# Kernel optimization log

Hardware: AMD Instinct MI355X
Metric: run time of the kernel (lower is better)

The kernel has to match this reference:

```python
import jax, jax.numpy as jnp
import numpy as np

N = 50000
E = 800000
EPS = 1e-5
GAT_SLOPE = 0.2   # PyG GATConv internal LeakyReLU slope
ACT_SLOPE = 0.01  # decoder's LeakyReLU(alpha)


def setup_inputs() -> dict:
    key = jax.random.key(0)
    ks = jax.random.split(key, 10)
    d = {
        "embeddings": jax.random.normal(ks[0], (N, 64), jnp.float32),
        "edge_index": jax.random.randint(ks[1], (2, E), 0, N, jnp.int64),
        "W1": jax.random.normal(ks[2], (64, 128), jnp.float32) * 0.1,
        "a_src1": jax.random.normal(ks[3], (128,), jnp.float32) * 0.1,
        "a_dst1": jax.random.normal(ks[4], (128,), jnp.float32) * 0.1,
        "b1": jnp.zeros((128,), jnp.float32),
        "gamma1": jnp.ones((128,), jnp.float32),
        "beta1": jnp.zeros((128,), jnp.float32),
        "W2": jax.random.normal(ks[5], (128, 256), jnp.float32) * 0.1,
        "a_src2": jax.random.normal(ks[6], (256,), jnp.float32) * 0.1,
        "a_dst2": jax.random.normal(ks[7], (256,), jnp.float32) * 0.1,
        "b2": jnp.zeros((256,), jnp.float32),
        "gamma2": jnp.ones((256,), jnp.float32),
        "beta2": jnp.zeros((256,), jnp.float32),
        "Wf": jax.random.normal(ks[8], (256, 256), jnp.float32) * 0.1,
        "bf": jnp.zeros((256,), jnp.float32),
    }
    return d


def gat_conv(x, src, dst, W, a_s, a_d, b):
    # PyG GATConv, heads=1, concat=False, add_self_loops=True (loops appended in caller)
    h = x @ W                                    # [N, out]
    e = h @ a_s                                  # alpha_src per node
    f = h @ a_d                                  # alpha_dst per node
    logits = jax.nn.leaky_relu(e[src] + f[dst], GAT_SLOPE)   # [E']
    # scatter-softmax over destination neighborhoods
    m = jax.ops.segment_max(logits, dst, num_segments=N)
    ex = jnp.exp(logits - m[dst])
    denom = jax.ops.segment_sum(ex, dst, num_segments=N)
    alpha = ex / denom[dst]                      # [E']
    out = jax.ops.segment_sum(h[src] * alpha[:, None], dst, num_segments=N)
    return out + b


def batch_norm(x, gamma, beta):
    mu = jnp.mean(x, axis=0)
    var = jnp.mean((x - mu) ** 2, axis=0)        # biased, as torch BN uses
    return (x - mu) * jax.lax.rsqrt(var + EPS) * gamma + beta


def reference(embeddings, edge_index, W1, a_src1, a_dst1, b1, gamma1, beta1,
              W2, a_src2, a_dst2, b2, gamma2, beta2, Wf, bf):
    loops = jnp.arange(N, dtype=edge_index.dtype)
    src = jnp.concatenate([edge_index[0], loops])
    dst = jnp.concatenate([edge_index[1], loops])
    x = embeddings
    for (W, a_s, a_d, b, g, be) in [
        (W1, a_src1, a_dst1, b1, gamma1, beta1),
        (W2, a_src2, a_dst2, b2, gamma2, beta2),
    ]:
        x = gat_conv(x, src, dst, W, a_s, a_d, b)
        x = batch_norm(x, g, be)
        x = jax.nn.leaky_relu(x, ACT_SLOPE)
        # dropout: identity (eval mode)
    return x @ Wf + bf
```

## Files before the change

### kernel.cpp

```cpp
#include <hip/hip_runtime.h>
#include <hip/hip_fp16.h>
#include <math.h>

#define N_NODES 50000
#define N_EDGES 800000
#define N_TOT   850000
#define EPS_BN  1e-5f
#define GAT_SLOPE 0.2f
#define ACT_SLOPE 0.01f
#define NBUCK   ((N_NODES + 255) / 256)
#define BCAP    5120
#define K1_CH   4096
#define K1_NB   ((N_TOT + K1_CH - 1) / K1_CH)
#define GB64    ((N_NODES + 63) / 64)

typedef _Float16 half8_t __attribute__((ext_vector_type(8)));
typedef _Float16 half4_t __attribute__((ext_vector_type(4)));
typedef _Float16 half2_t __attribute__((ext_vector_type(2)));
typedef float    f32x4   __attribute__((ext_vector_type(4)));

__device__ __forceinline__ float wred_max(float x) {
#pragma unroll
    for (int m = 32; m; m >>= 1) x = fmaxf(x, __shfl_xor(x, m, 64));
    return x;
}
__device__ __forceinline__ float wred_sum(float x) {
#pragma unroll
    for (int m = 32; m; m >>= 1) x += __shfl_xor(x, m, 64);
    return x;
}
__device__ __forceinline__ int wred_sum_i(int x) {
#pragma unroll
    for (int m = 32; m; m >>= 1) x += __shfl_xor(x, m, 64);
    return x;
}

__device__ __forceinline__ void store_val(float* p, float v) { *p = v; }
__device__ __forceinline__ void store_val(_Float16* p, float v) { *p = (_Float16)v; }

__global__ void init_misc(const float* __restrict__ W1, const float* __restrict__ W2,
                          const float* __restrict__ Wf, _Float16* __restrict__ wt1,
                          _Float16* __restrict__ wt2, _Float16* __restrict__ wtf,
                          int* __restrict__ bcnt,
                          const float* __restrict__ as1, const float* __restrict__ ad1,
                          const float* __restrict__ as2, const float* __restrict__ ad2,
                          float* __restrict__ va1, float* __restrict__ vb1,
                          float* __restrict__ va2, float* __restrict__ vb2) {
    int i = blockIdx.x * 256 + threadIdx.x;
    if (i < NBUCK) bcnt[i] = 0;
    if (i < 8192) {
        int k = i >> 7, c = i & 127;
        wt1[c * 64 + k] = (_Float16)W1[i];
    } else if (i < 8192 + 32768) {
        int j = i - 8192, k = j >> 8, c = j & 255;
        wt2[c * 128 + k] = (_Float16)W2[j];
    } else if (i < 8192 + 32768 + 65536) {
        int j = i - 40960, k = j >> 8, c = j & 255;
        wtf[c * 256 + k] = (_Float16)Wf[j];
    } else if (i < 106496 + 384) {
        int j = i - 106496;
        if (j < 64) {
            float s = 0.f;
            for (int c = 0; c < 128; ++c) s += W1[j * 128 + c] * as1[c];
            va1[j] = s;
        } else if (j < 128) {
            int k = j - 64; float s = 0.f;
            for (int c = 0; c < 128; ++c) s += W1[k * 128 + c] * ad1[c];
            vb1[k] = s;
        } else if (j < 256) {
            int k = j - 128; float s = 0.f;
            for (int c = 0; c < 256; ++c) s += W2[k * 256 + c] * as2[c];
            va2[k] = s;
        } else {
            int k = j - 256; float s = 0.f;
            for (int c = 0; c < 256; ++c) s += W2[k * 256 + c] * ad2[c];
            vb2[k] = s;
        }
    }
}

__global__ __launch_bounds__(256) void
emb_dots(const float* __restrict__ emb, const float* __restrict__ va,
         const float* __restrict__ vb, _Float16* __restrict__ embh,
         float* __restrict__ e_n, float* __restrict__ f_n) {
    int r = blockIdx.x * 4 + (threadIdx.x >> 6);
    if (r >= N_NODES) return;
    int l = threadIdx.x & 63;
    float v = emb[(size_t)r * 64 + l];
    embh[(size_t)r * 64 + l] = (_Float16)v;
    float pe = wred_sum(v * va[l]);
    float pf = wred_sum(v * vb[l]);
    if (l == 0) { e_n[r] = pe; f_n[r] = pf; }
}

__global__ __launch_bounds__(256) void
ef_dots(const _Float16* __restrict__ x, const float* __restrict__ sc,
        const float* __restrict__ sh, const float* __restrict__ va,
        const float* __restrict__ vb, _Float16* __restrict__ z,
        float* __restrict__ e_n, float* __restrict__ f_n) {
    int r = blockIdx.x * 4 + (threadIdx.x >> 6);
    if (r >= N_NODES) return;
    int l = threadIdx.x & 63;
    int c = 2 * l;
    half2_t hv = *(const half2_t*)&x[(size_t)r * 128 + c];
    float x0 = (float)hv[0] * sc[c] + sh[c];
    float x1 = (float)hv[1] * sc[c + 1] + sh[c + 1];
    x0 = x0 > 0.f ? x0 : ACT_SLOPE * x0;
    x1 = x1 > 0.f ? x1 : ACT_SLOPE * x1;
    half2_t zo = { (_Float16)x0, (_Float16)x1 };
    *(half2_t*)&z[(size_t)r * 128 + c] = zo;
    float pe = wred_sum(x0 * va[c] + x1 * va[c + 1]);
    float pf = wred_sum(x0 * vb[c] + x1 * vb[c + 1]);
    if (l == 0) { e_n[r] = pe; f_n[r] = pf; }
}

template<int K, int C, typename InT, typename OutT, bool STATS>
__global__ __launch_bounds__(256) void
gemm_mfma(const InT* __restrict__ x, const _Float16* __restrict__ wt,
          const float* __restrict__ bias, OutT* __restrict__ out, int n,
          const float* __restrict__ scale, const float* __restrict__ shift,
          float2* __restrict__ pbn) {
    constexpr int NW_C = C / 64;
    constexpr int RT   = NW_C;
    constexpr int LK   = K + 8;
    __shared__ _Float16 xs[64 * LK];
    __shared__ float cs_sh[STATS ? C : 1];
    __shared__ float cq_sh[STATS ? C : 1];
    const int row0 = blockIdx.x * 64;
    const int t = threadIdx.x;

    if (STATS) {
        for (int c = t; c < C; c += 256) { cs_sh[c] = 0.f; cq_sh[c] = 0.f; }
    }

    if constexpr (__is_same(InT, _Float16)) {
        for (int i = t * 8; i < 64 * K; i += 256 * 8) {
            int r = i / K, c = i - (i / K) * K;
            half8_t v = {};
            if (row0 + r < n) v = *(const half8_t*)&x[(size_t)(row0 + r) * K + c];
            if (scale) {
#pragma unroll
                for (int j = 0; j < 8; ++j) {
                    float f = (float)v[j] * scale[c + j] + shift[c + j];
                    v[j] = (_Float16)(f > 0.f ? f : ACT_SLOPE * f);
                }
            }
            *(half8_t*)&xs[r * LK + c] = v;
        }
    } else {
        for (int i = t * 4; i < 64 * K; i += 256 * 4) {
            int r = i / K, c = i - (i / K) * K;
            float4 v = make_float4(0.f, 0.f, 0.f, 0.f);
            if (row0 + r < n) v = *(const float4*)&x[(size_t)(row0 + r) * K + c];
            if (scale) {
                v.x = v.x * scale[c] + shift[c];         v.x = v.x > 0.f ? v.x : ACT_SLOPE * v.x;
                v.y = v.y * scale[c + 1] + shift[c + 1]; v.y = v.y > 0.f ? v.y : ACT_SLOPE * v.y;
                v.z = v.z * scale[c + 2] + shift[c + 2]; v.z = v.z > 0.f ? v.z : ACT_SLOPE * v.z;
                v.w = v.w * scale[c + 3] + shift[c + 3]; v.w = v.w > 0.f ? v.w : ACT_SLOPE * v.w;
            }
            half4_t h4 = { (_Float16)v.x, (_Float16)v.y, (_Float16)v.z, (_Float16)v.w };
            *(half4_t*)&xs[r * LK + c] = h4;
        }
    }
    __syncthreads();

    const int w = t >> 6, l = t & 63;
    const int l16 = l & 15, quad = l >> 4;
    const int c0 = (w % NW_C) * 64;
    const int mbase = (w / NW_C) * (16 * NW_C);

    f32x4 acc[RT][4] = {};
    for (int k0 = 0; k0 < K; k0 += 32) {
        half8_t b[4];
#pragma unroll
        for (int tt = 0; tt < 4; ++tt)
            b[tt] = *(const half8_t*)&wt[(size_t)(c0 + tt * 16 + l16) * K + k0 + quad * 8];
        half8_t a[RT];
#pragma unroll
        for (int rt = 0; rt < RT; ++rt)
            a[rt] = *(const half8_t*)&xs[(mbase + rt * 16 + l16) * LK + k0 + quad * 8];
#pragma unroll
        for (int rt = 0; rt < RT; ++rt)
#pragma unroll
            for (int tt = 0; tt < 4; ++tt)
                acc[rt][tt] = __builtin_amdgcn_mfma_f32_16x16x32_f16(a[rt], b[tt],
                                                                     acc[rt][tt], 0, 0, 0);
    }

#pragma unroll
    for (int rt = 0; rt < RT; ++rt) {
        int rb = row0 + mbase + rt * 16 + quad * 4;
#pragma unroll
        for (int tt = 0; tt < 4; ++tt) {
            int col = c0 + tt * 16 + l16;
            float bb = bias ? bias[col] : 0.f;
#pragma unroll
            for (int i = 0; i < 4; ++i)
                if (rb + i < n)
                    store_val(&out[(size_t)(rb + i) * C + col], acc[rt][tt][i] + bb);
        }
    }

    if constexpr (STATS) {
#pragma unroll
        for (int tt = 0; tt < 4; ++tt) {
            int col = c0 + tt * 16 + l16;
            float bb = bias ? bias[col] : 0.f;
            float s = 0.f, q = 0.f;
#pragma unroll
            for (int rt = 0; rt < RT; ++rt) {
                int rb = row0 + mbase + rt * 16 + quad * 4;
#pragma unroll
                for (int i = 0; i < 4; ++i) {
                    if (rb + i < n) {
                        float v = acc[rt][tt][i] + bb;
                        s += v; q += v * v;
                    }
                }
            }
            s += __shfl_xor(s, 16, 64); s += __shfl_xor(s, 32, 64);
            q += __shfl_xor(q, 16, 64); q += __shfl_xor(q, 32, 64);
            if (quad == 0) {
                atomicAdd(&cs_sh[col], s);
                atomicAdd(&cq_sh[col], q);
            }
        }
        __syncthreads();
        for (int c = t; c < C; c += 256)
            pbn[(size_t)blockIdx.x * C + c] = make_float2(cs_sh[c], cq_sh[c]);
    }
}

__global__ __launch_bounds__(256) void
bucket_append(const int* __restrict__ ei, int* __restrict__ bcnt,
              unsigned* __restrict__ bedge) {
    __shared__ int lcnt[NBUCK], lrank[NBUCK], gbase[NBUCK];
    const int t = threadIdx.x;
    const int base = blockIdx.x * K1_CH;
    const int nE = min(K1_CH, N_TOT - base);
    for (int i = t; i < NBUCK; i += 256) { lcnt[i] = 0; lrank[i] = 0; }
    __syncthreads();
    for (int i = t; i < nE; i += 256) {
        int e = base + i;
        int d = (e < N_EDGES) ? ei[N_EDGES + e] : (e - N_EDGES);
        atomicAdd(&lcnt[d >> 8], 1);
    }
    __syncthreads();
    if (t < NBUCK && lcnt[t] > 0) gbase[t] = atomicAdd(&bcnt[t], lcnt[t]);
    __syncthreads();
    for (int i = t; i < nE; i += 256) {
        int e = base + i;
        int s, d;
        if (e < N_EDGES) { s = ei[e]; d = ei[N_EDGES + e]; }
        else { s = e - N_EDGES; d = s; }
        int bk = d >> 8;
        int gp = gbase[bk] + atomicAdd(&lrank[bk], 1);
        if (gp < BCAP)
            bedge[(size_t)bk * BCAP + gp] = ((unsigned)d << 16) | (unsigned)s;
    }
}

__global__ __launch_bounds__(256) void
bucket_csr(const int* __restrict__ bcnt, const unsigned* __restrict__ bedge,
           int* __restrict__ ptr, int* __restrict__ srcs) {
    __shared__ int lcnt[256], lptr[256], lrank[256];
    __shared__ int wsum[4];
    __shared__ int sbase;
    const int b = blockIdx.x, t = threadIdx.x;
    lcnt[t] = 0; lrank[t] = 0;
    if (t < 64) {
        int s = 0;
        for (int j = t; j < b; j += 64) s += bcnt[j];
        s = wred_sum_i(s);
        if (t == 0) sbase = s;
    }
    __syncthreads();
    const int cnt = min(bcnt[b], BCAP);
    const int base0 = sbase;
    const unsigned* eb = bedge + (size_t)b * BCAP;
    for (int i = t; i < cnt; i += 256) atomicAdd(&lcnt[(eb[i] >> 16) & 255], 1);
    __syncthreads();
    int lane = t & 63, w = t >> 6;
    int v = lcnt[t];
    int x = v;
#pragma unroll
    for (int off = 1; off < 64; off <<= 1) {
        int y = __shfl_up(x, off, 64);
        if (lane >= off) x += y;
    }
    if (lane == 63) wsum[w] = x;
    __syncthreads();
    if (t == 0) {
        int s = 0;
#pragma unroll
        for (int i = 0; i < 4; ++i) { int tmp = wsum[i]; wsum[i] = s; s += tmp; }
    }
    __syncthreads();
    lptr[t] = x - v + wsum[w];
    __syncthreads();
    int d = b * 256 + t;
    if (d < N_NODES) ptr[d] = base0 + lptr[t];
    if (b == NBUCK - 1 && t == 0) ptr[N_NODES] = base0 + cnt;
    for (int i = t; i < cnt; i += 256) {
        unsigned v2 = eb[i];
        int dl = (v2 >> 16) & 255;
        int pos = base0 + lptr[dl] + atomicAdd(&lrank[dl], 1);
        srcs[pos] = (int)(v2 & 0xFFFFu);
    }
}

template<int C>
__global__ __launch_bounds__(256) void
attn_aggregate(const _Float16* __restrict__ h, const int* __restrict__ srcs,
               const int* __restrict__ ptr, const float* __restrict__ e_n,
               const float* __restrict__ f_n, _Float16* __restrict__ out) {
    constexpr int RL = C / 8;
    constexpr int G  = 64 / RL;
    int d = blockIdx.x * 4 + (threadIdx.x >> 6);
    if (d >= N_NODES) return;
    int l  = threadIdx.x & 63;
    int b0 = ptr[d], b1 = ptr[d + 1];
    int deg = b1 - b0;
    float fd = f_n[d];
    const int g  = l / RL;
    const int cl = l % RL;
    float acc[8] = {0.f, 0.f, 0.f, 0.f, 0.f, 0.f, 0.f, 0.f};

    if (deg <= 64) {
        int sj = 0; float lg = -1e30f;
        if (l < deg) {
            sj = srcs[b0 + l];
            float v = e_n[sj] + fd;
            lg = v > 0.f ? v : GAT_SLOPE * v;
        }
        float m  = wred_max(lg);
        float e0 = (l < deg) ? __expf(lg - m) : 0.f;
        float ex = e0 / wred_sum(e0);

        int jj = 0;
        for (; jj + 4 * G <= deg; jj += 4 * G) {
            float wk[4]; int sk[4];
#pragma unroll
            for (int k = 0; k < 4; ++k) {
                int j = jj + k * G + g;
                wk[k] = __shfl(ex, j, 64);
                sk[k] = __shfl(sj, j, 64);
            }
            half8_t v[4];
#pragma unroll
            for (int k = 0; k < 4; ++k)
                v[k] = *(const half8_t*)&h[(size_t)sk[k] * C + cl * 8];
#pragma unroll
            for (int k = 0; k < 4; ++k)
#pragma unroll
                for (int i = 0; i < 8; ++i)
                    acc[i] += wk[k] * (float)v[k][i];
        }
        for (; jj + 2 * G <= deg; jj += 2 * G) {
            float w1 = __shfl(ex, jj + g, 64);
            int   s1 = __shfl(sj, jj + g, 64);
            float w2 = __shfl(ex, jj + G + g, 64);
            int   s2 = __shfl(sj, jj + G + g, 64);
            half8_t v1 = *(const half8_t*)&h[(size_t)s1 * C + cl * 8];
            half8_t v2 = *(const half8_t*)&h[(size_t)s2 * C + cl * 8];
#pragma unroll
            for (int i = 0; i < 8; ++i)
                acc[i] += w1 * (float)v1[i] + w2 * (float)v2[i];
        }
        for (; jj < deg; jj += G) {
            int j = jj + g;
            float wk = __shfl(ex, j, 64);
            int   sk = __shfl(sj, j, 64);
            if (j < deg) {
                half8_t v = *(const half8_t*)&h[(size_t)sk * C + cl * 8];
#pragma unroll
                for (int i = 0; i < 8; ++i) acc[i] += wk * (float)v[i];
            }
        }
    } else {
        float m_l = -1e30f, den_l = 0.f;
        for (int j = b0 + l; j < b1; j += 64) {
            float lg = e_n[srcs[j]] + fd;
            lg = lg > 0.f ? lg : GAT_SLOPE * lg;
            float nm = fmaxf(m_l, lg);
            den_l = den_l * __expf(m_l - nm) + __expf(lg - nm);
            m_l = nm;
        }
        float m = wred_max(m_l);
        float inv = 1.f / wred_sum(den_l * __expf(m_l - m));
        for (int c0 = b0; c0 < b1; c0 += 64) {
            int jl = c0 + l;
            int sj = 0; float ex = 0.f;
            if (jl < b1) {
                sj = srcs[jl];
                float lg = e_n[sj] + fd;
                lg = lg > 0.f ? lg : GAT_SLOPE * lg;
                ex = __expf(lg - m) * inv;
            }
            int nE = min(64, b1 - c0);
            for (int jj = 0; jj < nE; jj += 2 * G) {
                int j1 = jj + g, j2 = jj + G + g;
                float w1 = __shfl(ex, j1, 64);
                int   s1 = __shfl(sj, j1, 64);
                float w2 = __shfl(ex, j2, 64);
                int   s2 = __shfl(sj, j2, 64);
                half8_t v1 = *(const half8_t*)&h[(size_t)s1 * C + cl * 8];
                half8_t v2 = *(const half8_t*)&h[(size_t)s2 * C + cl * 8];
#pragma unroll
                for (int i = 0; i < 8; ++i)
                    acc[i] += w1 * (float)v1[i] + w2 * (float)v2[i];
            }
        }
    }
#pragma unroll
    for (int mm = RL; mm < 64; mm <<= 1)
#pragma unroll
        for (int i = 0; i < 8; ++i) acc[i] += __shfl_xor(acc[i], mm, 64);
    if (g == 0) {
        int c = cl * 8;
        half8_t o;
#pragma unroll
        for (int i = 0; i < 8; ++i) o[i] = (_Float16)acc[i];
        *(half8_t*)&out[(size_t)d * C + c] = o;
    }
}

template<int C, int PB>
__global__ __launch_bounds__(256) void
bn_coef(const float2* __restrict__ partial, const float* __restrict__ gamma,
        const float* __restrict__ beta, float* __restrict__ scale,
        float* __restrict__ shift) {
    int w = threadIdx.x >> 6, l = threadIdx.x & 63;
    int c = blockIdx.x * 4 + w;
    float s = 0.f, q = 0.f;
    for (int b = l; b < PB; b += 64) {
        float2 p = partial[(size_t)b * C + c];
        s += p.x; q += p.y;
    }
    s = wred_sum(s); q = wred_sum(q);
    if (l == 0) {
        float mu  = s / N_NODES;
        float var = q / N_NODES - mu * mu;
        float sc = gamma[c] * rsqrtf(var + EPS_BN);
        scale[c] = sc;
        shift[c] = beta[c] - mu * sc;
    }
}

extern "C" void kernel_launch(void* const* d_in, const int* in_sizes, int n_in,
                              void* d_out, int out_size, void* d_ws, size_t ws_size,
                              hipStream_t stream) {
    const float* emb  = (const float*)d_in[0];
    const int*   ei   = (const int*)  d_in[1];
    const float* W1   = (const float*)d_in[2];
    const float* as1  = (const float*)d_in[3];
    const float* ad1  = (const float*)d_in[4];
    const float* b1   = (const float*)d_in[5];
    const float* g1   = (const float*)d_in[6];
    const float* be1  = (const float*)d_in[7];
    const float* W2   = (const float*)d_in[8];
    const float* as2  = (const float*)d_in[9];
    const float* ad2  = (const float*)d_in[10];
    const float* b2   = (const float*)d_in[11];
    const float* g2   = (const float*)d_in[12];
    const float* be2  = (const float*)d_in[13];
    const float* Wf   = (const float*)d_in[14];
    const float* bf   = (const float*)d_in[15];
    float* out = (float*)d_out;

    char* w = (char*)d_ws;
    auto alloc = [&](size_t bytes) {
        char* p = w;
        w += (bytes + 255) & ~(size_t)255;
        return (void*)p;
    };
    _Float16* embh = (_Float16*)alloc((size_t)N_NODES * 64 * 2);
    _Float16* agg1 = (_Float16*)alloc((size_t)N_NODES * 64 * 2);
    _Float16* out1 = (_Float16*)alloc((size_t)N_NODES * 128 * 2);
    _Float16* agg2 = (_Float16*)alloc((size_t)N_NODES * 128 * 2);
    _Float16* out2 = (_Float16*)alloc((size_t)N_NODES * 256 * 2);
    _Float16* z1h  = embh;
    unsigned* bedge = (unsigned*)out2;
    float*  e_n  = (float*) alloc((size_t)N_NODES * 4);
    float*  f_n  = (float*) alloc((size_t)N_NODES * 4);
    int*    srcs = (int*)   alloc((size_t)N_TOT * 4);
    int*    bcnt = (int*)   alloc((size_t)NBUCK * 4);
    int*    ptr  = (int*)   alloc((size_t)(N_NODES + 1) * 4);
    float2* pbn  = (float2*)alloc((size_t)GB64 * 256 * 8);
    float*  sc1  = (float*) alloc(128 * 4);
    float*  sh1  = (float*) alloc(128 * 4);
    float*  sc2  = (float*) alloc(256 * 4);
    float*  sh2  = (float*) alloc(256 * 4);
    float*  va1  = (float*) alloc(64 * 4);
    float*  vb1  = (float*) alloc(64 * 4);
    float*  va2  = (float*) alloc(128 * 4);
    float*  vb2  = (float*) alloc(128 * 4);
    _Float16* wt1 = (_Float16*)alloc((size_t)64 * 128 * 2);
    _Float16* wt2 = (_Float16*)alloc((size_t)128 * 256 * 2);
    _Float16* wtf = (_Float16*)alloc((size_t)256 * 256 * 2);

    const int RW4 = (N_NODES + 3) / 4;

    init_misc<<<(106496 + 384 + 255) / 256, 256, 0, stream>>>(
        W1, W2, Wf, wt1, wt2, wtf, bcnt, as1, ad1, as2, ad2, va1, vb1, va2, vb2);

    emb_dots<<<RW4, 256, 0, stream>>>(emb, va1, vb1, embh, e_n, f_n);

    bucket_append<<<K1_NB, 256, 0, stream>>>(ei, bcnt, bedge);
    bucket_csr<<<NBUCK, 256, 0, stream>>>(bcnt, bedge, ptr, srcs);

    attn_aggregate<64><<<RW4, 256, 0, stream>>>(embh, srcs, ptr, e_n, f_n, agg1);
    gemm_mfma<64, 128, _Float16, _Float16, true><<<GB64, 256, 0, stream>>>(
        agg1, wt1, b1, out1, N_NODES, nullptr, nullptr, pbn);
    bn_coef<128, GB64><<<128 / 4, 256, 0, stream>>>(pbn, g1, be1, sc1, sh1);

    ef_dots<<<RW4, 256, 0, stream>>>(out1, sc1, sh1, va2, vb2, z1h, e_n, f_n);
    attn_aggregate<128><<<RW4, 256, 0, stream>>>(z1h, srcs, ptr, e_n, f_n, agg2);
    gemm_mfma<128, 256, _Float16, _Float16, true><<<GB64, 256, 0, stream>>>(
        agg2, wt2, b2, out2, N_NODES, nullptr, nullptr, pbn);
    bn_coef<256, GB64><<<256 / 4, 256, 0, stream>>>(pbn, g2, be2, sc2, sh2);

    gemm_mfma<256, 256, _Float16, float, false><<<GB64, 256, 0, stream>>>(
        out2, wtf, bf, out, N_NODES, sc2, sh2, nullptr);
}
```

Measured before the change: 318.6 us.

## Split GEMM columns across blocks, stage output through LDS, double-buffer weight loads

The MFMA GEMM kernel gains a column-block template parameter, so the 256-wide GEMMs launch twice as many blocks, each covering 128 columns. This raises parallelism and cuts per-wave accumulator count. Results are written to an LDS buffer that aliases the input tile, then stored to global memory as coalesced vector writes instead of scattered scalar stores. Weight fragments are double-buffered across k-steps to overlap global loads with MFMA. In exchange, the input tile is re-read and re-normalised once per column block, and two extra barriers are added.

```diff
diff --git a/kernel.cpp b/kernel.cpp
--- a/kernel.cpp
+++ b/kernel.cpp
@@ -34,9 +34,6 @@
     for (int m = 32; m; m >>= 1) x += __shfl_xor(x, m, 64);
     return x;
 }
-
-__device__ __forceinline__ void store_val(float* p, float v) { *p = v; }
-__device__ __forceinline__ void store_val(_Float16* p, float v) { *p = (_Float16)v; }
 
 __global__ void init_misc(const float* __restrict__ W1, const float* __restrict__ W2,
                           const float* __restrict__ Wf, _Float16* __restrict__ wt1,
@@ -114,23 +111,33 @@
     if (l == 0) { e_n[r] = pe; f_n[r] = pf; }
 }
 
-template<int K, int C, typename InT, typename OutT, bool STATS>
+template<int K, int C, int CB, typename InT, typename OutT, bool STATS>
 __global__ __launch_bounds__(256) void
 gemm_mfma(const InT* __restrict__ x, const _Float16* __restrict__ wt,
           const float* __restrict__ bias, OutT* __restrict__ out, int n,
           const float* __restrict__ scale, const float* __restrict__ shift,
           float2* __restrict__ pbn) {
-    constexpr int NW_C = C / 64;
+    constexpr int NW_C = CB / 64;
     constexpr int RT   = NW_C;
+    constexpr int NCB  = C / CB;
     constexpr int LK   = K + 8;
-    __shared__ _Float16 xs[64 * LK];
-    __shared__ float cs_sh[STATS ? C : 1];
-    __shared__ float cq_sh[STATS ? C : 1];
-    const int row0 = blockIdx.x * 64;
+    constexpr int LCB  = CB + 4;
+    constexpr size_t SMB = ((size_t)64 * LK * 2 > (size_t)64 * LCB * 4)
+                             ? (size_t)64 * LK * 2 : (size_t)64 * LCB * 4;
+    __shared__ alignas(16) char smem[SMB];
+    _Float16* xs  = (_Float16*)smem;
+    float*   cbuf = (float*)smem;
+    __shared__ float cs_sh[STATS ? CB : 1];
+    __shared__ float cq_sh[STATS ? CB : 1];
+
+    const int rb = blockIdx.x / NCB;
+    const int cblk = blockIdx.x - rb * NCB;
+    const int row0 = rb * 64;
+    const int colB = cblk * CB;
     const int t = threadIdx.x;
 
     if (STATS) {
-        for (int c = t; c < C; c += 256) { cs_sh[c] = 0.f; cq_sh[c] = 0.f; }
+        for (int c = t; c < CB; c += 256) { cs_sh[c] = 0.f; cq_sh[c] = 0.f; }
     }
 
     if constexpr (__is_same(InT, _Float16)) {
@@ -166,15 +173,18 @@
 
     const int w = t >> 6, l = t & 63;
     const int l16 = l & 15, quad = l >> 4;
-    const int c0 = (w % NW_C) * 64;
+    const int lc0 = (w % NW_C) * 64;
+    const int gc0 = colB + lc0;
     const int mbase = (w / NW_C) * (16 * NW_C);
 
     f32x4 acc[RT][4] = {};
-    for (int k0 = 0; k0 < K; k0 += 32) {
-        half8_t b[4];
+    half8_t bA[4], bB[4];
+    auto loadB = [&](int k0, half8_t* bf) {
 #pragma unroll
         for (int tt = 0; tt < 4; ++tt)
-            b[tt] = *(const half8_t*)&wt[(size_t)(c0 + tt * 16 + l16) * K + k0 + quad * 8];
+            bf[tt] = *(const half8_t*)&wt[(size_t)(gc0 + tt * 16 + l16) * K + k0 + quad * 8];
+    };
+    auto doMM = [&](int k0, half8_t* bf) {
         half8_t a[RT];
 #pragma unroll
         for (int rt = 0; rt < RT; ++rt)
@@ -183,51 +193,60 @@
         for (int rt = 0; rt < RT; ++rt)
 #pragma unroll
             for (int tt = 0; tt < 4; ++tt)
-                acc[rt][tt] = __builtin_amdgcn_mfma_f32_16x16x32_f16(a[rt], b[tt],
+                acc[rt][tt] = __builtin_amdgcn_mfma_f32_16x16x32_f16(a[rt], bf[tt],
                                                                      acc[rt][tt], 0, 0, 0);
-    }
-
+    };
+    loadB(0, bA);
+#pragma unroll
+    for (int k0 = 0; k0 < K; k0 += 64) {
+        loadB(k0 + 32, bB);
+        doMM(k0, bA);
+        if (k0 + 64 < K) loadB(k0 + 64, bA);
+        doMM(k0 + 32, bB);
+    }
+
+    __syncthreads();
 #pragma unroll
     for (int rt = 0; rt < RT; ++rt) {
-        int rb = row0 + mbase + rt * 16 + quad * 4;
 #pragma unroll
         for (int tt = 0; tt < 4; ++tt) {
-            int col = c0 + tt * 16 + l16;
-            float bb = bias ? bias[col] : 0.f;
-#pragma unroll
-            for (int i = 0; i < 4; ++i)
-                if (rb + i < n)
-                    store_val(&out[(size_t)(rb + i) * C + col], acc[rt][tt][i] + bb);
-        }
-    }
-
+            int lcol = lc0 + tt * 16 + l16;
+            float bb = bias ? bias[colB + lcol] : 0.f;
+            float s = 0.f, q = 0.f;
+#pragma unroll
+            for (int i = 0; i < 4; ++i) {
+                int lrow = mbase + rt * 16 + quad * 4 + i;
+                float v = acc[rt][tt][i] + bb;
+                cbuf[lrow * LCB + lcol] = v;
+                if (STATS && row0 + lrow < n) { s += v; q += v * v; }
+            }
+            if constexpr (STATS) {
+                s += __shfl_xor(s, 16, 64); s += __shfl_xor(s, 32, 64);
+                q += __shfl_xor(q, 16, 64); q += __shfl_xor(q, 32, 64);
+                if (quad == 0) {
+                    atomicAdd(&cs_sh[lcol], s);
+                    atomicAdd(&cq_sh[lcol], q);
+                }
+            }
+        }
+    }
+    __syncthreads();
     if constexpr (STATS) {
-#pragma unroll
-        for (int tt = 0; tt < 4; ++tt) {
-            int col = c0 + tt * 16 + l16;
-            float bb = bias ? bias[col] : 0.f;
-            float s = 0.f, q = 0.f;
-#pragma unroll
-            for (int rt = 0; rt < RT; ++rt) {
-                int rb = row0 + mbase + rt * 16 + quad * 4;
-#pragma unroll
-                for (int i = 0; i < 4; ++i) {
-                    if (rb + i < n) {
-                        float v = acc[rt][tt][i] + bb;
-                        s += v; q += v * v;
-                    }
-                }
-            }
-            s += __shfl_xor(s, 16, 64); s += __shfl_xor(s, 32, 64);
-            q += __shfl_xor(q, 16, 64); q += __shfl_xor(q, 32, 64);
-            if (quad == 0) {
-                atomicAdd(&cs_sh[col], s);
-                atomicAdd(&cq_sh[col], q);
-            }
-        }
-        __syncthreads();
-        for (int c = t; c < C; c += 256)
-            pbn[(size_t)blockIdx.x * C + c] = make_float2(cs_sh[c], cq_sh[c]);
+        for (int c = t; c < CB; c += 256)
+            pbn[(size_t)rb * C + colB + c] = make_float2(cs_sh[c], cq_sh[c]);
+    }
+    for (int i = t * 4; i < 64 * CB; i += 256 * 4) {
+        int r = i / CB, c = i - (i / CB) * CB;
+        if (row0 + r < n) {
+            float4 v4 = *(const float4*)&cbuf[r * LCB + c];
+            if constexpr (__is_same(OutT, float)) {
+                *(float4*)&out[(size_t)(row0 + r) * C + colB + c] = v4;
+            } else {
+                half4_t h4 = { (_Float16)v4.x, (_Float16)v4.y,
+                               (_Float16)v4.z, (_Float16)v4.w };
+                *(half4_t*)&out[(size_t)(row0 + r) * C + colB + c] = h4;
+            }
+        }
     }
 }
 
@@ -510,16 +529,16 @@
     bucket_csr<<<NBUCK, 256, 0, stream>>>(bcnt, bedge, ptr, srcs);
 
     attn_aggregate<64><<<RW4, 256, 0, stream>>>(embh, srcs, ptr, e_n, f_n, agg1);
-    gemm_mfma<64, 128, _Float16, _Float16, true><<<GB64, 256, 0, stream>>>(
+    gemm_mfma<64, 128, 128, _Float16, _Float16, true><<<GB64, 256, 0, stream>>>(
         agg1, wt1, b1, out1, N_NODES, nullptr, nullptr, pbn);
     bn_coef<128, GB64><<<128 / 4, 256, 0, stream>>>(pbn, g1, be1, sc1, sh1);
 
     ef_dots<<<RW4, 256, 0, stream>>>(out1, sc1, sh1, va2, vb2, z1h, e_n, f_n);
     attn_aggregate<128><<<RW4, 256, 0, stream>>>(z1h, srcs, ptr, e_n, f_n, agg2);
-    gemm_mfma<128, 256, _Float16, _Float16, true><<<GB64, 256, 0, stream>>>(
+    gemm_mfma<128, 256, 128, _Float16, _Float16, true><<<GB64 * 2, 256, 0, stream>>>(
         agg2, wt2, b2, out2, N_NODES, nullptr, nullptr, pbn);
     bn_coef<256, GB64><<<256 / 4, 256, 0, stream>>>(pbn, g2, be2, sc2, sh2);
 
-    gemm_mfma<256, 256, _Float16, float, false><<<GB64, 256, 0, stream>>>(
+    gemm_mfma<256, 256, 128, _Float16, float, false><<<GB64 * 2, 256, 0, stream>>>(
         out2, wtf, bf, out, N_NODES, sc2, sh2, nullptr);
 }
```

Result: no change. 317.1 us (-0.5%).
